# Performance work log

Hardware: AMD Instinct MI355X
Metric: run time of the kernel (lower is better)

## Reference

```python
import jax, jax.numpy as jnp
import numpy as np

B, S, D, H = 2, 2048, 1024, 16
HD = D // H  # head_dim = 64
ROPE_BASE = 10000.0


def apply_rope(x, positions):
    # x: [B, S, H, HD], positions: [B, S] int. Rotate-half RoPE.
    d = x.shape[-1]
    inv_freq = 1.0 / (ROPE_BASE ** (jnp.arange(0, d, 2, dtype=jnp.float32) / d))  # [d/2]
    ang = positions[..., None].astype(jnp.float32) * inv_freq  # [B, S, d/2]
    cos = jnp.cos(ang)[:, :, None, :]
    sin = jnp.sin(ang)[:, :, None, :]
    x1, x2 = jnp.split(x, 2, axis=-1)
    return jnp.concatenate([x1 * cos - x2 * sin, x2 * cos + x1 * sin], axis=-1).astype(x.dtype)


def setup_inputs() -> dict:
    key = jax.random.key(0)
    k1, k2, k3 = jax.random.split(key, 3)
    inputs = jax.random.normal(k1, (B, S, D), dtype=jnp.float32)
    # nn.Linear weights [out_features, in_features]
    W_in = jax.random.normal(k2, (3 * D, D), dtype=jnp.float32) * (1.0 / np.sqrt(D))
    W_out = jax.random.normal(k3, (D, D), dtype=jnp.float32) * (1.0 / np.sqrt(D))
    positions = jnp.tile(jnp.arange(S, dtype=jnp.int32)[None, :], (B, 1))  # [B, S]
    return {"inputs": inputs, "positions": positions, "W_in": W_in, "W_out": W_out}


def reference(inputs, positions, W_in, W_out):
    # fused QKV projection: [B, S, 3D], head-major layout per rearrange '(heads qkv)'
    qkv = jnp.einsum('bsd,ed->bse', inputs, W_in)
    qkv = qkv.reshape(B, S, H, 3 * HD)
    q, k, v = jnp.split(qkv, 3, axis=-1)  # each [B, S, H, HD]
    q = apply_rope(q, positions)
    k = apply_rope(k, positions)
    # einsum_attention (inference path): scale query, full masked softmax
    q = q / jnp.sqrt(jnp.asarray(HD, dtype=q.dtype))
    scores = jnp.einsum('bqhd,bkhd->bhqk', q, k)  # [B, H, S, S]
    mask = (jnp.arange(S)[None, None, :] <= positions[:, :, None])[:, None, :, :]  # [B,1,S,S]
    big_neg = jnp.finfo(scores.dtype).min
    scores = jnp.where(mask, scores, big_neg)
    attn = jax.nn.softmax(scores, axis=-1)
    x = jnp.einsum('bhqk,bkhd->bqhd', attn, v).reshape(B, S, D)
    return jnp.einsum('bsd,ed->bse', x, W_out)
```

## Files before the change

### kernel.cpp

```cpp
#include <hip/hip_runtime.h>
#include <stdint.h>
#include <math.h>

#define B_ 2
#define S_ 2048
#define D_ 1024
#define H_ 16
#define HD_ 64
#define KVBLK 64

typedef __bf16 bf16_t;
typedef __bf16 bf16x4 __attribute__((ext_vector_type(4)));
typedef __bf16 bf16x8 __attribute__((ext_vector_type(8)));
typedef float f32x4 __attribute__((ext_vector_type(4)));
typedef float f32x16 __attribute__((ext_vector_type(16)));
typedef float float4v __attribute__((ext_vector_type(4)));

#define L2E 1.4426950408889634f
#define NINF (-__builtin_inff())

__device__ __forceinline__ void gload_lds16(const bf16_t* g, bf16_t* l) {
  __builtin_amdgcn_global_load_lds((const __attribute__((address_space(1))) void*)g,
                                   (__attribute__((address_space(3))) void*)l, 16, 0, 0);
}

__device__ __forceinline__ uint32_t packbf(float a, float b) {
  union { __bf16 h[2]; uint32_t u; } cvt;
  cvt.h[0] = (__bf16)a; cvt.h[1] = (__bf16)b;
  return cvt.u;
}

__global__ void cast3_bf16_kernel(const float* __restrict__ s0, bf16_t* __restrict__ d0, int n0,
                                  const float* __restrict__ s1, bf16_t* __restrict__ d1, int n1,
                                  const float* __restrict__ s2, bf16_t* __restrict__ d2, int n2) {
  int i = blockIdx.x * blockDim.x + threadIdx.x;
  int stride = gridDim.x * blockDim.x;
  int tot = n0 + n1 + n2;
  for (; i < tot; i += stride) {
    const float* s; bf16_t* d; int j = i;
    if (j < n0) { s = s0; d = d0; }
    else if ((j -= n0) < n1) { s = s1; d = d1; }
    else { j -= n1; s = s2; d = d2; }
    float4v f = *(const float4v*)(s + (size_t)j * 4);
    bf16x4 o;
    o[0] = (__bf16)f[0]; o[1] = (__bf16)f[1]; o[2] = (__bf16)f[2]; o[3] = (__bf16)f[3];
    *(bf16x4*)(d + (size_t)j * 4) = o;
  }
}

template <typename OutT>
__global__ __launch_bounds__(256) void gemm_bt(const bf16_t* __restrict__ A,
                                               const bf16_t* __restrict__ Bm,
                                               OutT* __restrict__ C,
                                               int M, int N, int K) {
  __shared__ bf16_t As[128 * 32];
  __shared__ bf16_t Bs[128 * 32];
  const int t = threadIdx.x;
  const int lane = t & 63, wave = t >> 6;
  const int wr = wave >> 1, wc = wave & 1;
  const int qr = lane & 15, g = lane >> 4;
  const int bm = blockIdx.x, bn = blockIdx.y;

  f32x4 acc[4][4];
#pragma unroll
  for (int m = 0; m < 4; m++)
#pragma unroll
    for (int n = 0; n < 4; n++) acc[m][n] = (f32x4){0.f, 0.f, 0.f, 0.f};

  const bf16_t* Abase = A + (size_t)(bm * 128) * K;
  const bf16_t* Bbase = Bm + (size_t)(bn * 128) * K;
  const int srow = t >> 2;
  const int scol = (t & 3) * 8;

  for (int kk = 0; kk < K; kk += 32) {
    gload_lds16(Abase + (size_t)srow * K + kk + scol,        As + t * 8);
    gload_lds16(Abase + (size_t)(srow + 64) * K + kk + scol, As + 2048 + t * 8);
    gload_lds16(Bbase + (size_t)srow * K + kk + scol,        Bs + t * 8);
    gload_lds16(Bbase + (size_t)(srow + 64) * K + kk + scol, Bs + 2048 + t * 8);
    __syncthreads();
    bf16x8 a[4], b[4];
#pragma unroll
    for (int m = 0; m < 4; m++)
      a[m] = *(const bf16x8*)(As + (wr * 64 + m * 16 + qr) * 32 + g * 8);
#pragma unroll
    for (int n = 0; n < 4; n++)
      b[n] = *(const bf16x8*)(Bs + (wc * 64 + n * 16 + qr) * 32 + g * 8);
#pragma unroll
    for (int m = 0; m < 4; m++)
#pragma unroll
      for (int n = 0; n < 4; n++)
        acc[m][n] = __builtin_amdgcn_mfma_f32_16x16x32_bf16(a[m], b[n], acc[m][n], 0, 0, 0);
    __syncthreads();
  }

#pragma unroll
  for (int m = 0; m < 4; m++) {
    int row0 = bm * 128 + wr * 64 + m * 16 + g * 4;
#pragma unroll
    for (int n = 0; n < 4; n++) {
      int col = bn * 128 + wc * 64 + n * 16 + qr;
#pragma unroll
      for (int r = 0; r < 4; r++)
        C[(size_t)(row0 + r) * N + col] = (OutT)acc[m][n][r];
    }
  }
}

template <typename OutT>
__global__ __launch_bounds__(512, 2) void gemm256(const bf16_t* __restrict__ A,
                                                  const bf16_t* __restrict__ Bm,
                                                  OutT* __restrict__ C,
                                                  int M, int N, int K) {
  __shared__ bf16_t As[2][256 * 64];
  __shared__ bf16_t Bs[2][256 * 64];
  const int t = threadIdx.x;
  const int lane = t & 63, wid = t >> 6;
  const int qr = lane & 15, g = lane >> 4;
  const int wm = wid >> 2, wn = wid & 3;
  const int bm = blockIdx.x, bn = blockIdx.y;
  const int NT = K >> 6;

  const bf16_t* Ab = A + (size_t)(bm * 256) * K;
  const bf16_t* Bb = Bm + (size_t)(bn * 256) * K;

  const bf16_t* srcA[4];
  const bf16_t* srcB[4];
  int ldsOff[4];
#pragma unroll
  for (int i = 0; i < 4; i++) {
    int e = t + 512 * i;
    int row = e >> 3, cs = e & 7;
    int gcol = (cs ^ (row & 7)) * 8;
    srcA[i] = Ab + (size_t)row * K + gcol;
    srcB[i] = Bb + (size_t)row * K + gcol;
    ldsOff[i] = e * 8;
  }

  f32x4 acc[8][4];
#pragma unroll
  for (int m = 0; m < 8; m++)
#pragma unroll
    for (int n = 0; n < 4; n++) acc[m][n] = (f32x4){0.f, 0.f, 0.f, 0.f};

#define RD(buf_, r_, k_) (*(const bf16x8*)((buf_) + (r_) * 64 + ((((k_) * 4 + g) ^ ((r_) & 7)) * 8)))

#pragma unroll
  for (int i = 0; i < 4; i++) gload_lds16(srcA[i], As[0] + ldsOff[i]);
#pragma unroll
  for (int i = 0; i < 4; i++) gload_lds16(srcB[i], Bs[0] + ldsOff[i]);
#pragma unroll
  for (int i = 0; i < 4; i++) gload_lds16(srcA[i] + 64, As[1] + ldsOff[i]);
#pragma unroll
  for (int i = 0; i < 4; i++) gload_lds16(srcB[i] + 64, Bs[1] + ldsOff[i]);

  for (int T = 0; T < NT; ++T) {
    bf16_t* A_c = As[T & 1];
    bf16_t* B_c = Bs[T & 1];
    if (T + 1 < NT) asm volatile("s_waitcnt vmcnt(8)" ::: "memory");
    else            asm volatile("s_waitcnt vmcnt(0)" ::: "memory");
    __builtin_amdgcn_sched_barrier(0);
    __builtin_amdgcn_s_barrier();

    const bool st = (T + 2 < NT);
    const int kt2 = (T + 2) * 64;

    bf16x8 alo[4][2], ahi[4][2], bfr[4][2];

#pragma unroll
    for (int m = 0; m < 4; m++) {
      int r = wm * 128 + m * 16 + qr;
      alo[m][0] = RD(A_c, r, 0); alo[m][1] = RD(A_c, r, 1);
    }
#pragma unroll
    for (int n = 0; n < 2; n++) {
      int r = wn * 64 + n * 16 + qr;
      bfr[n][0] = RD(B_c, r, 0); bfr[n][1] = RD(B_c, r, 1);
    }
    __builtin_amdgcn_s_barrier();
    __builtin_amdgcn_s_setprio(1);
#pragma unroll
    for (int m = 0; m < 4; m++)
#pragma unroll
      for (int n = 0; n < 2; n++)
#pragma unroll
        for (int k = 0; k < 2; k++)
          acc[m][n] = __builtin_amdgcn_mfma_f32_16x16x32_bf16(alo[m][k], bfr[n][k], acc[m][n], 0, 0, 0);
    __builtin_amdgcn_s_setprio(0);
    __builtin_amdgcn_s_barrier();

#pragma unroll
    for (int n = 2; n < 4; n++) {
      int r = wn * 64 + n * 16 + qr;
      bfr[n][0] = RD(B_c, r, 0); bfr[n][1] = RD(B_c, r, 1);
    }
    if (st) {
      gload_lds16(srcA[0] + kt2, A_c + ldsOff[0]);
      gload_lds16(srcA[2] + kt2, A_c + ldsOff[2]);
    }
    __builtin_amdgcn_s_barrier();
    __builtin_amdgcn_s_setprio(1);
#pragma unroll
    for (int m = 0; m < 4; m++)
#pragma unroll
      for (int n = 2; n < 4; n++)
#pragma unroll
        for (int k = 0; k < 2; k++)
          acc[m][n] = __builtin_amdgcn_mfma_f32_16x16x32_bf16(alo[m][k], bfr[n][k], acc[m][n], 0, 0, 0);
    __builtin_amdgcn_s_setprio(0);
    __builtin_amdgcn_s_barrier();

#pragma unroll
    for (int m = 0; m < 4; m++) {
      int r = wm * 128 + (m + 4) * 16 + qr;
      ahi[m][0] = RD(A_c, r, 0); ahi[m][1] = RD(A_c, r, 1);
    }
    if (st) {
      gload_lds16(srcB[0] + kt2, B_c + ldsOff[0]);
      gload_lds16(srcB[1] + kt2, B_c + ldsOff[1]);
      gload_lds16(srcB[2] + kt2, B_c + ldsOff[2]);
      gload_lds16(srcB[3] + kt2, B_c + ldsOff[3]);
    }
    __builtin_amdgcn_s_barrier();
    __builtin_amdgcn_s_setprio(1);
#pragma unroll
    for (int m = 0; m < 4; m++)
#pragma unroll
      for (int n = 0; n < 2; n++)
#pragma unroll
        for (int k = 0; k < 2; k++)
          acc[m + 4][n] = __builtin_amdgcn_mfma_f32_16x16x32_bf16(ahi[m][k], bfr[n][k], acc[m + 4][n], 0, 0, 0);
    __builtin_amdgcn_s_setprio(0);
    __builtin_amdgcn_s_barrier();

    if (st) {
      gload_lds16(srcA[1] + kt2, A_c + ldsOff[1]);
      gload_lds16(srcA[3] + kt2, A_c + ldsOff[3]);
    }
    __builtin_amdgcn_s_barrier();
    __builtin_amdgcn_s_setprio(1);
#pragma unroll
    for (int m = 0; m < 4; m++)
#pragma unroll
      for (int n = 2; n < 4; n++)
#pragma unroll
        for (int k = 0; k < 2; k++)
          acc[m + 4][n] = __builtin_amdgcn_mfma_f32_16x16x32_bf16(ahi[m][k], bfr[n][k], acc[m + 4][n], 0, 0, 0);
    __builtin_amdgcn_s_setprio(0);
    __builtin_amdgcn_s_barrier();
  }
#undef RD

#pragma unroll
  for (int m = 0; m < 8; m++) {
    int row0 = bm * 256 + wm * 128 + m * 16 + g * 4;
#pragma unroll
    for (int n = 0; n < 4; n++) {
      int col = bn * 256 + wn * 64 + n * 16 + qr;
#pragma unroll
      for (int r = 0; r < 4; r++)
        C[(size_t)(row0 + r) * N + col] = (OutT)acc[m][n][r];
    }
  }
}

__global__ void rope_qk_kernel(const bf16_t* __restrict__ qkv, const int* __restrict__ pos,
                               bf16_t* __restrict__ Q, bf16_t* __restrict__ Ko) {
  int idx = blockIdx.x * blockDim.x + threadIdx.x;
  if (idx >= B_ * S_ * H_ * 32) return;
  int i = idx & 31;
  int h = (idx >> 5) & (H_ - 1);
  int bs = idx >> 9;
  const bf16_t* row = qkv + (size_t)bs * (3 * D_) + h * 192;
  float q1 = (float)row[i], q2 = (float)row[i + 32];
  float k1 = (float)row[64 + i], k2 = (float)row[96 + i];
  int p = pos[bs];
  float inv = exp2f(-(float)i * (13.287712379549449f / 32.0f));
  float ang = (float)p * inv;
  float sn, cs;
  sincosf(ang, &sn, &cs);
  float qo1 = (q1 * cs - q2 * sn) * 0.125f;
  float qo2 = (q2 * cs + q1 * sn) * 0.125f;
  float ko1 = k1 * cs - k2 * sn;
  float ko2 = k2 * cs + k1 * sn;
  int b = bs >> 11, s = bs & (S_ - 1);
  size_t o = ((size_t)(b * H_ + h) * S_ + s) * HD_ + i;
  Q[o] = (__bf16)qo1;  Q[o + 32] = (__bf16)qo2;
  Ko[o] = (__bf16)ko1; Ko[o + 32] = (__bf16)ko2;
}

__global__ __launch_bounds__(256) void v_transpose_kernel(const bf16_t* __restrict__ qkv,
                                                          bf16_t* __restrict__ Vt) {
  __shared__ bf16_t tile[64][72];
  int t = threadIdx.x;
  int s0 = blockIdx.x * 64;
  int h = blockIdx.y, b = blockIdx.z;
  int sl = t >> 4;
  int cb = (t & 15) * 4;
#pragma unroll
  for (int it = 0; it < 4; it++) {
    int s = sl + it * 16;
    const bf16_t* src = qkv + (size_t)(b * S_ + s0 + s) * (3 * D_) + h * 192 + 128 + cb;
    bf16x4 v = *(const bf16x4*)src;
    tile[cb + 0][s] = v[0]; tile[cb + 1][s] = v[1];
    tile[cb + 2][s] = v[2]; tile[cb + 3][s] = v[3];
  }
  __syncthreads();
#pragma unroll
  for (int it = 0; it < 4; it++) {
    int d = sl + it * 16;
    bf16x4 v;
    v[0] = tile[d][cb]; v[1] = tile[d][cb + 1]; v[2] = tile[d][cb + 2]; v[3] = tile[d][cb + 3];
    *(bf16x4*)(Vt + ((size_t)((b * H_ + h) * HD_ + d)) * S_ + s0 + cb) = v;
  }
}

__global__ __launch_bounds__(256) void attn_kernel(const bf16_t* __restrict__ Q,
                                                   const bf16_t* __restrict__ K,
                                                   const bf16_t* __restrict__ Vt,
                                                   const int* __restrict__ pos,
                                                   bf16_t* __restrict__ O,
                                                   bf16_t* __restrict__ Opart,
                                                   float* __restrict__ Mst,
                                                   float* __restrict__ Lst) {
  __shared__ bf16_t Ks[2][64 * 64];
  __shared__ bf16_t Vs[2][64 * 64];

  const int t = threadIdx.x;
  const int lane = t & 63, wv = t >> 6;
  const int l31 = lane & 31, hi = lane >> 5;

  const int bid = blockIdx.x;
  const int bh = (bid & 7) * 4 + ((bid >> 3) & 3);
  const int v5 = bid >> 5;
  const int qblk = 15 - (v5 >> 1);
  const int half = v5 & 1;
  const int b = bh >> 4, h = bh & 15;
  const int q0 = qblk * 128;

  const bf16_t* Qb = Q + (size_t)bh * (S_ * HD_);
  const bf16_t* Kb = K + (size_t)bh * (S_ * HD_);
  const bf16_t* Vb = Vt + (size_t)bh * (HD_ * S_);

  const int qrow = q0 + wv * 32 + l31;

  const int prow = pos[b * S_ + qrow];
  int wmin = prow;
#pragma unroll
  for (int off = 1; off < 32; off <<= 1) wmin = min(wmin, __shfl_xor(wmin, off));

  int mp = max(pos[b * S_ + q0 + lane], pos[b * S_ + q0 + 64 + lane]);
#pragma unroll
  for (int off = 1; off < 64; off <<= 1) mp = max(mp, __shfl_xor(mp, off));
  const int nt = min(S_ / KVBLK, (mp >> 6) + 1);

  const int t0 = half * 16;
  const int t1 = min(nt, t0 + 16);
  if (t0 >= t1) return;
  const bool needs_merge = (nt > 16);

  bf16x8 qf[4];
#pragma unroll
  for (int c = 0; c < 4; c++)
    qf[c] = *(const bf16x8*)(Qb + (size_t)qrow * HD_ + c * 16 + hi * 8);

  const int r0 = t >> 3, c0 = t & 7;
  const int r1 = (t + 256) >> 3, c1 = t & 7;
  const bf16_t* KgA = Kb + (size_t)r0 * HD_ + ((c0 ^ (r0 & 7)) * 8);
  const bf16_t* KgB = Kb + (size_t)r1 * HD_ + ((c1 ^ (r1 & 7)) * 8);
  const bf16_t* VgA = Vb + (size_t)r0 * S_ + ((c0 ^ (r0 & 7)) * 8);
  const bf16_t* VgB = Vb + (size_t)r1 * S_ + ((c1 ^ (r1 & 7)) * 8);
  const int ldsA = t * 8, ldsB = (t + 256) * 8;

  f32x16 oT[2];
#pragma unroll
  for (int dt = 0; dt < 2; dt++)
#pragma unroll
    for (int r = 0; r < 16; r++) oT[dt][r] = 0.f;
  float m_run = NINF, l_run = 0.f;

  {
    const int kn = t0 * KVBLK;
    gload_lds16(KgA + (size_t)kn * HD_, Ks[0] + ldsA);
    gload_lds16(KgB + (size_t)kn * HD_, Ks[0] + ldsB);
    gload_lds16(VgA + kn, Vs[0] + ldsA);
    gload_lds16(VgB + kn, Vs[0] + ldsB);
  }
  __syncthreads();

  for (int kt = t0; kt < t1; ++kt) {
    const int k0 = kt * KVBLK;
    const int cur = kt & 1;
    if (kt + 1 < t1) {
      const int kn = (kt + 1) * KVBLK;
      gload_lds16(KgA + (size_t)kn * HD_, Ks[cur ^ 1] + ldsA);
      gload_lds16(KgB + (size_t)kn * HD_, Ks[cur ^ 1] + ldsB);
      gload_lds16(VgA + kn, Vs[cur ^ 1] + ldsA);
      gload_lds16(VgB + kn, Vs[cur ^ 1] + ldsB);
    }
    const bf16_t* Kc = Ks[cur];
    const bf16_t* Vc = Vs[cur];

    f32x16 s0, s1;
#pragma unroll
    for (int r = 0; r < 16; r++) { s0[r] = 0.f; s1[r] = 0.f; }
    __builtin_amdgcn_s_setprio(1);
#pragma unroll
    for (int c = 0; c < 4; c++) {
      const int c2 = c * 2 + hi;
      const int kr0 = l31;
      const int kr1 = 32 + l31;
      bf16x8 kf0 = *(const bf16x8*)(Kc + kr0 * 64 + ((c2 ^ (kr0 & 7)) * 8));
      bf16x8 kf1 = *(const bf16x8*)(Kc + kr1 * 64 + ((c2 ^ (kr1 & 7)) * 8));
      s0 = __builtin_amdgcn_mfma_f32_32x32x16_bf16(kf0, qf[c], s0, 0, 0, 0);
      s1 = __builtin_amdgcn_mfma_f32_32x32x16_bf16(kf1, qf[c], s1, 0, 0, 0);
    }
    __builtin_amdgcn_s_setprio(0);

    float p0[16], p1[16];
    if (k0 + 63 > wmin) {
#pragma unroll
      for (int r = 0; r < 16; r++) {
        int koff = (r & 3) + 8 * (r >> 2) + 4 * hi;
        p0[r] = (k0 + koff <= prow) ? s0[r] : NINF;
        p1[r] = (k0 + 32 + koff <= prow) ? s1[r] : NINF;
      }
    } else {
#pragma unroll
      for (int r = 0; r < 16; r++) { p0[r] = s0[r]; p1[r] = s1[r]; }
    }

    float tm = NINF;
#pragma unroll
    for (int r = 0; r < 16; r++) tm = fmaxf(tm, fmaxf(p0[r], p1[r]));
    tm = fmaxf(tm, __shfl_xor(tm, 32));
    if (__any(tm > m_run + 8.0f)) {
      float mn = fmaxf(fmaxf(m_run, tm), -1e30f);
      float scale = exp2f((m_run - mn) * L2E);
      l_run *= scale;
#pragma unroll
      for (int dt = 0; dt < 2; dt++)
#pragma unroll
        for (int r = 0; r < 16; r++) oT[dt][r] *= scale;
      m_run = mn;
    }
    const float mnl = (m_run == NINF) ? 3.0e38f : m_run * L2E;
    float rs = 0.f;
#pragma unroll
    for (int r = 0; r < 16; r++) {
      p0[r] = exp2f(p0[r] * L2E - mnl);
      p1[r] = exp2f(p1[r] * L2E - mnl);
      rs += p0[r] + p1[r];
    }
    rs += __shfl_xor(rs, 32);
    l_run += rs;

#pragma unroll
    for (int kc = 0; kc < 4; kc++) {
      const float* P = (kc < 2) ? p0 : p1;
      const int rb = (kc & 1) * 8;
      uint32_t xa0 = packbf(P[rb + 0], P[rb + 1]);
      uint32_t xa1 = packbf(P[rb + 2], P[rb + 3]);
      uint32_t xb0 = packbf(P[rb + 4], P[rb + 5]);
      uint32_t xb1 = packbf(P[rb + 6], P[rb + 7]);
      uint32_t sa0 = (uint32_t)__shfl_xor((int)xa0, 32);
      uint32_t sa1 = (uint32_t)__shfl_xor((int)xa1, 32);
      uint32_t sb0 = (uint32_t)__shfl_xor((int)xb0, 32);
      uint32_t sb1 = (uint32_t)__shfl_xor((int)xb1, 32);
      union { uint32_t u[4]; bf16x8 v; } pf;
      pf.u[0] = hi ? sb0 : xa0;
      pf.u[1] = hi ? sb1 : xa1;
      pf.u[2] = hi ? xb0 : sa0;
      pf.u[3] = hi ? xb1 : sa1;
      __builtin_amdgcn_s_setprio(1);
#pragma unroll
      for (int dt = 0; dt < 2; dt++) {
        const int vr = dt * 32 + l31;
        const int c2 = kc * 2 + hi;
        bf16x8 vf = *(const bf16x8*)(Vc + vr * 64 + ((c2 ^ (vr & 7)) * 8));
        oT[dt] = __builtin_amdgcn_mfma_f32_32x32x16_bf16(vf, pf.v, oT[dt], 0, 0, 0);
      }
      __builtin_amdgcn_s_setprio(0);
    }

    __syncthreads();
  }

  const float rl = needs_merge ? 1.0f : ((l_run > 0.f) ? 1.0f / l_run : 0.f);
  bf16_t* Ot = (bf16_t*)Ks + wv * 2048;
#pragma unroll
  for (int dt = 0; dt < 2; dt++)
#pragma unroll
    for (int r = 0; r < 16; r++) {
      int chunk = dt * 4 + (r >> 2);
      int el = (r & 3) + 4 * hi;
      Ot[l31 * 64 + ((chunk ^ (l31 & 7)) * 8) + el] = (__bf16)(oT[dt][r] * rl);
    }
  __syncthreads();
  if (needs_merge) {
    bf16_t* dst = Opart + (((size_t)(half * 32 + bh) * 16 + qblk) * 128) * 64;
#pragma unroll
    for (int it = 0; it < 4; it++) {
      int qr2 = (lane >> 3) + it * 8;
      int cc = lane & 7;
      bf16x8 vv = *(const bf16x8*)(Ot + qr2 * 64 + ((cc ^ (qr2 & 7)) * 8));
      *(bf16x8*)(&dst[(size_t)(wv * 32 + qr2) * 64 + cc * 8]) = vv;
    }
    if (hi == 0) {
      size_t sidx = ((size_t)(half * 32 + bh) * 16 + qblk) * 128 + wv * 32 + l31;
      Mst[sidx] = m_run;
      Lst[sidx] = l_run;
    }
  } else {
#pragma unroll
    for (int it = 0; it < 4; it++) {
      int qr2 = (lane >> 3) + it * 8;
      int cc = lane & 7;
      bf16x8 vv = *(const bf16x8*)(Ot + qr2 * 64 + ((cc ^ (qr2 & 7)) * 8));
      *(bf16x8*)(&O[(size_t)(b * S_ + q0 + wv * 32 + qr2) * D_ + h * 64 + cc * 8]) = vv;
    }
  }
}

__global__ __launch_bounds__(256) void attn_merge_kernel(const bf16_t* __restrict__ Opart,
                                                         const float* __restrict__ Mst,
                                                         const float* __restrict__ Lst,
                                                         const int* __restrict__ pos,
                                                         bf16_t* __restrict__ O) {
  __shared__ int wmax_s[4];
  const int t = threadIdx.x;
  const int bid = blockIdx.x;
  const int bh = (bid & 7) * 4 + ((bid >> 3) & 3);
  const int qblk = 15 - (bid >> 5);
  const int b = bh >> 4, h = bh & 15;
  const int q0 = qblk * 128;

  int p = pos[b * S_ + q0 + (t & 127)];
#pragma unroll
  for (int off = 1; off < 64; off <<= 1) p = max(p, __shfl_xor(p, off));
  if ((t & 63) == 0) wmax_s[t >> 6] = p;
  __syncthreads();
  int mp = max(max(wmax_s[0], wmax_s[1]), max(wmax_s[2], wmax_s[3]));
  if ((mp >> 6) + 1 <= 16) return;

  const int r = t >> 1, dh = (t & 1) * 32;
  const size_t s0i = ((size_t)(0 * 32 + bh) * 16 + qblk) * 128 + r;
  const size_t s1i = ((size_t)(1 * 32 + bh) * 16 + qblk) * 128 + r;
  float m0 = Mst[s0i], l0 = Lst[s0i];
  float m1 = Mst[s1i], l1 = Lst[s1i];
  float m = fmaxf(fmaxf(m0, m1), -1e30f);
  float w0 = exp2f((m0 - m) * L2E);
  float w1 = exp2f((m1 - m) * L2E);
  float lt = l0 * w0 + l1 * w1;
  float rl = (lt > 0.f) ? 1.0f / lt : 0.f;
  w0 *= rl; w1 *= rl;
  const bf16_t* pa = Opart + s0i * 64 + dh;
  const bf16_t* pb = Opart + s1i * 64 + dh;
  bf16_t* dst = O + (size_t)(b * S_ + q0 + r) * D_ + h * 64 + dh;
#pragma unroll
  for (int c = 0; c < 4; c++) {
    bf16x8 a = *(const bf16x8*)(pa + c * 8);
    bf16x8 bb = *(const bf16x8*)(pb + c * 8);
    bf16x8 o;
#pragma unroll
    for (int j = 0; j < 8; j++)
      o[j] = (__bf16)((float)a[j] * w0 + (float)bb[j] * w1);
    *(bf16x8*)(dst + c * 8) = o;
  }
}

extern "C" void kernel_launch(void* const* d_in, const int* in_sizes, int n_in,
                              void* d_out, int out_size, void* d_ws, size_t ws_size,
                              hipStream_t stream) {
  const float* inputs = (const float*)d_in[0];
  const int* positions = (const int*)d_in[1];
  const float* W_in = (const float*)d_in[2];
  const float* W_out = (const float*)d_in[3];
  float* out = (float*)d_out;

  bf16_t* X_bf = (bf16_t*)d_ws;
  bf16_t* Win_bf = X_bf + (size_t)4096 * 1024;
  bf16_t* Wout_bf = Win_bf + (size_t)3072 * 1024;
  bf16_t* qkv_bf = Wout_bf + (size_t)1024 * 1024;
  bf16_t* Qb = qkv_bf + (size_t)4096 * 3072;
  bf16_t* Kb = Qb + (size_t)B_ * H_ * S_ * HD_;
  bf16_t* Vtb = Kb + (size_t)B_ * H_ * S_ * HD_;
  bf16_t* Ob = Vtb + (size_t)B_ * H_ * S_ * HD_;

  bf16_t* Opart = qkv_bf;
  float* Mst = (float*)(qkv_bf + (size_t)2 * 32 * 16 * 128 * 64);
  float* Lst = Mst + (size_t)2 * 32 * 16 * 128;

  cast3_bf16_kernel<<<dim3(2048), dim3(256), 0, stream>>>(
      inputs, X_bf, (4096 * 1024) / 4,
      W_in, Win_bf, (3072 * 1024) / 4,
      W_out, Wout_bf, (1024 * 1024) / 4);

  gemm256<bf16_t><<<dim3(16, 12), dim3(512), 0, stream>>>(X_bf, Win_bf, qkv_bf, 4096, 3072, 1024);

  rope_qk_kernel<<<dim3((B_ * S_ * H_ * 32) / 256), dim3(256), 0, stream>>>(qkv_bf, positions, Qb, Kb);
  v_transpose_kernel<<<dim3(S_ / 64, H_, B_), dim3(256), 0, stream>>>(qkv_bf, Vtb);

  attn_kernel<<<dim3(1024), dim3(256), 0, stream>>>(Qb, Kb, Vtb, positions, Ob, Opart, Mst, Lst);
  attn_merge_kernel<<<dim3(512), dim3(256), 0, stream>>>(Opart, Mst, Lst, positions, Ob);

  gemm_bt<float><<<dim3(32, 8), dim3(256), 0, stream>>>(Ob, Wout_bf, out, 4096, 1024, 1024);
}
```

Baseline: 152.9 us.

## Fuse RoPE and V transpose into the QKV projection GEMM epilogue

The QKV GEMM epilogue now writes Q (RoPE-rotated and scaled), K (RoPE-rotated) and transposed V straight into their attention layouts, using the fact that each 64-column wave tile maps to one head's q, k or v slice. This removes the intermediate qkv buffer round trip and two extra kernel launches. In exchange the epilogue computes sincos per element and issues scattered 2-byte or strided 8-byte stores. Launch bounds also drop from 2 to 1 blocks per CU, which may change register allocation.

```diff
diff --git a/kernel.cpp b/kernel.cpp
--- a/kernel.cpp
+++ b/kernel.cpp
@@ -106,11 +106,14 @@
   }
 }
 
-template <typename OutT>
-__global__ __launch_bounds__(512, 2) void gemm256(const bf16_t* __restrict__ A,
-                                                  const bf16_t* __restrict__ Bm,
-                                                  OutT* __restrict__ C,
-                                                  int M, int N, int K) {
+__global__ __launch_bounds__(512, 1) void gemm_qkv_rope(const bf16_t* __restrict__ A,
+                                                        const bf16_t* __restrict__ Bm,
+                                                        const int* __restrict__ pos,
+                                                        bf16_t* __restrict__ Qd,
+                                                        bf16_t* __restrict__ Kd,
+                                                        bf16_t* __restrict__ Vtd) {
+  const int K = D_;
+  const int NT = K >> 6;
   __shared__ bf16_t As[2][256 * 64];
   __shared__ bf16_t Bs[2][256 * 64];
   const int t = threadIdx.x;
@@ -118,7 +121,6 @@
   const int qr = lane & 15, g = lane >> 4;
   const int wm = wid >> 2, wn = wid & 3;
   const int bm = blockIdx.x, bn = blockIdx.y;
-  const int NT = K >> 6;
 
   const bf16_t* Ab = A + (size_t)(bm * 256) * K;
   const bf16_t* Bb = Bm + (size_t)(bn * 256) * K;
@@ -250,67 +252,55 @@
   }
 #undef RD
 
-#pragma unroll
-  for (int m = 0; m < 8; m++) {
-    int row0 = bm * 256 + wm * 128 + m * 16 + g * 4;
-#pragma unroll
-    for (int n = 0; n < 4; n++) {
-      int col = bn * 256 + wn * 64 + n * 16 + qr;
-#pragma unroll
-      for (int r = 0; r < 4; r++)
-        C[(size_t)(row0 + r) * N + col] = (OutT)acc[m][n][r];
-    }
-  }
-}
-
-__global__ void rope_qk_kernel(const bf16_t* __restrict__ qkv, const int* __restrict__ pos,
-                               bf16_t* __restrict__ Q, bf16_t* __restrict__ Ko) {
-  int idx = blockIdx.x * blockDim.x + threadIdx.x;
-  if (idx >= B_ * S_ * H_ * 32) return;
-  int i = idx & 31;
-  int h = (idx >> 5) & (H_ - 1);
-  int bs = idx >> 9;
-  const bf16_t* row = qkv + (size_t)bs * (3 * D_) + h * 192;
-  float q1 = (float)row[i], q2 = (float)row[i + 32];
-  float k1 = (float)row[64 + i], k2 = (float)row[96 + i];
-  int p = pos[bs];
-  float inv = exp2f(-(float)i * (13.287712379549449f / 32.0f));
-  float ang = (float)p * inv;
-  float sn, cs;
-  sincosf(ang, &sn, &cs);
-  float qo1 = (q1 * cs - q2 * sn) * 0.125f;
-  float qo2 = (q2 * cs + q1 * sn) * 0.125f;
-  float ko1 = k1 * cs - k2 * sn;
-  float ko2 = k2 * cs + k1 * sn;
-  int b = bs >> 11, s = bs & (S_ - 1);
-  size_t o = ((size_t)(b * H_ + h) * S_ + s) * HD_ + i;
-  Q[o] = (__bf16)qo1;  Q[o + 32] = (__bf16)qo2;
-  Ko[o] = (__bf16)ko1; Ko[o + 32] = (__bf16)ko2;
-}
-
-__global__ __launch_bounds__(256) void v_transpose_kernel(const bf16_t* __restrict__ qkv,
-                                                          bf16_t* __restrict__ Vt) {
-  __shared__ bf16_t tile[64][72];
-  int t = threadIdx.x;
-  int s0 = blockIdx.x * 64;
-  int h = blockIdx.y, b = blockIdx.z;
-  int sl = t >> 4;
-  int cb = (t & 15) * 4;
-#pragma unroll
-  for (int it = 0; it < 4; it++) {
-    int s = sl + it * 16;
-    const bf16_t* src = qkv + (size_t)(b * S_ + s0 + s) * (3 * D_) + h * 192 + 128 + cb;
-    bf16x4 v = *(const bf16x4*)src;
-    tile[cb + 0][s] = v[0]; tile[cb + 1][s] = v[1];
-    tile[cb + 2][s] = v[2]; tile[cb + 3][s] = v[3];
-  }
-  __syncthreads();
-#pragma unroll
-  for (int it = 0; it < 4; it++) {
-    int d = sl + it * 16;
-    bf16x4 v;
-    v[0] = tile[d][cb]; v[1] = tile[d][cb + 1]; v[2] = tile[d][cb + 2]; v[3] = tile[d][cb + 3];
-    *(bf16x4*)(Vt + ((size_t)((b * H_ + h) * HD_ + d)) * S_ + s0 + cb) = v;
+  const int w = bn * 4 + wn;
+  const int typ = w % 3;
+  const int head = w / 3;
+
+  if (typ == 2) {
+#pragma unroll
+    for (int m = 0; m < 8; m++) {
+      int row0 = bm * 256 + wm * 128 + m * 16 + g * 4;
+      int b = row0 >> 11, s = row0 & (S_ - 1);
+#pragma unroll
+      for (int n = 0; n < 4; n++) {
+        int d = n * 16 + qr;
+        bf16x4 o;
+        o[0] = (__bf16)acc[m][n][0]; o[1] = (__bf16)acc[m][n][1];
+        o[2] = (__bf16)acc[m][n][2]; o[3] = (__bf16)acc[m][n][3];
+        *(bf16x4*)(Vtd + ((size_t)((b * H_ + head) * HD_ + d)) * S_ + s) = o;
+      }
+    }
+  } else {
+    bf16_t* dstb = (typ == 0) ? Qd : Kd;
+    const float qs = (typ == 0) ? 0.125f : 1.0f;
+    const float l2r = 13.287712379549449f / 32.0f;
+    float inv[2];
+    inv[0] = exp2f(-(float)qr * l2r);
+    inv[1] = exp2f(-(float)(qr + 16) * l2r);
+#pragma unroll
+    for (int m = 0; m < 8; m++) {
+      int row0 = bm * 256 + wm * 128 + m * 16 + g * 4;
+      int b = row0 >> 11;
+      bf16_t* base = dstb + (size_t)(b * H_ + head) * S_ * HD_;
+#pragma unroll
+      for (int rr = 0; rr < 4; rr++) {
+        int row = row0 + rr;
+        int s = row & (S_ - 1);
+        float p = (float)pos[row];
+#pragma unroll
+        for (int n = 0; n < 2; n++) {
+          float ang = p * inv[n];
+          float sn, cs;
+          sincosf(ang, &sn, &cs);
+          float x1 = acc[m][n][rr], x2 = acc[m][n + 2][rr];
+          float o1 = (x1 * cs - x2 * sn) * qs;
+          float o2 = (x2 * cs + x1 * sn) * qs;
+          int d = n * 16 + qr;
+          base[(size_t)s * HD_ + d] = (__bf16)o1;
+          base[(size_t)s * HD_ + d + 32] = (__bf16)o2;
+        }
+      }
+    }
   }
 }
 
@@ -580,14 +570,14 @@
   bf16_t* X_bf = (bf16_t*)d_ws;
   bf16_t* Win_bf = X_bf + (size_t)4096 * 1024;
   bf16_t* Wout_bf = Win_bf + (size_t)3072 * 1024;
-  bf16_t* qkv_bf = Wout_bf + (size_t)1024 * 1024;
-  bf16_t* Qb = qkv_bf + (size_t)4096 * 3072;
+  bf16_t* scratch = Wout_bf + (size_t)1024 * 1024;
+  bf16_t* Qb = scratch + (size_t)4096 * 3072;
   bf16_t* Kb = Qb + (size_t)B_ * H_ * S_ * HD_;
   bf16_t* Vtb = Kb + (size_t)B_ * H_ * S_ * HD_;
   bf16_t* Ob = Vtb + (size_t)B_ * H_ * S_ * HD_;
 
-  bf16_t* Opart = qkv_bf;
-  float* Mst = (float*)(qkv_bf + (size_t)2 * 32 * 16 * 128 * 64);
+  bf16_t* Opart = scratch;
+  float* Mst = (float*)(scratch + (size_t)2 * 32 * 16 * 128 * 64);
   float* Lst = Mst + (size_t)2 * 32 * 16 * 128;
 
   cast3_bf16_kernel<<<dim3(2048), dim3(256), 0, stream>>>(
@@ -595,10 +585,7 @@
       W_in, Win_bf, (3072 * 1024) / 4,
       W_out, Wout_bf, (1024 * 1024) / 4);
 
-  gemm256<bf16_t><<<dim3(16, 12), dim3(512), 0, stream>>>(X_bf, Win_bf, qkv_bf, 4096, 3072, 1024);
-
-  rope_qk_kernel<<<dim3((B_ * S_ * H_ * 32) / 256), dim3(256), 0, stream>>>(qkv_bf, positions, Qb, Kb);
-  v_transpose_kernel<<<dim3(S_ / 64, H_, B_), dim3(256), 0, stream>>>(qkv_bf, Vtb);
+  gemm_qkv_rope<<<dim3(16, 12), dim3(512), 0, stream>>>(X_bf, Win_bf, positions, Qb, Kb, Vtb);
 
   attn_kernel<<<dim3(1024), dim3(256), 0, stream>>>(Qb, Kb, Vtb, positions, Ob, Opart, Mst, Lst);
   attn_merge_kernel<<<dim3(512), dim3(256), 0, stream>>>(Opart, Mst, Lst, positions, Ob);
```

Measured after the change: 180.3 us. 17.9% more time.
